# Performance work log

Hardware: AMD Instinct MI355X
Metric: run time of the kernel (lower is better)

## Reference

```python
import jax, jax.numpy as jnp
import numpy as np

B = 16384       # batch
H = 512         # hidden_size
OUT = 4         # output_size (== GRU input_size)
FF = 2048       # MLP hidden width
HORIZON = 5     # prediction_horizon


def setup_inputs() -> dict:
    key = jax.random.key(0)
    ks = jax.random.split(key, 12)
    s = 0.05
    f32 = jnp.float32
    return {
        "predicted_values": jax.random.normal(ks[0], (B, HORIZON, OUT), f32),
        "past_time_features": jax.random.normal(ks[1], (B, H), f32),
        # nn.GRU (single layer) params, PyTorch layout: (3H, in) / (3H, H), gate order r,z,n
        "w_ih": jax.random.normal(ks[2], (3 * H, OUT), f32) * s,
        "w_hh": jax.random.normal(ks[3], (3 * H, H), f32) * s,
        "b_ih": jax.random.normal(ks[4], (3 * H,), f32) * s,
        "b_hh": jax.random.normal(ks[5], (3 * H,), f32) * s,
        # hx_fc: Linear(2H -> H)
        "w_fc": jax.random.normal(ks[6], (H, 2 * H), f32) * s,
        "b_fc": jax.random.normal(ks[7], (H,), f32) * s,
        # mlp: Linear(H -> 2048), Linear(2048 -> OUT); Dropout is identity at eval
        "w1": jax.random.normal(ks[8], (FF, H), f32) * s,
        "b1": jax.random.normal(ks[9], (FF,), f32) * s,
        "w2": jax.random.normal(ks[10], (OUT, FF), f32) * s,
        "b2": jax.random.normal(ks[11], (OUT,), f32) * s,
    }


def _gru_cell(x, h, w_ih, w_hh, b_ih, b_hh):
    # PyTorch GRU cell: gates ordered (r, z, n)
    gi = x @ w_ih.T + b_ih          # [B, 3H]
    gh = h @ w_hh.T + b_hh          # [B, 3H]
    i_r, i_z, i_n = jnp.split(gi, 3, axis=-1)
    h_r, h_z, h_n = jnp.split(gh, 3, axis=-1)
    r = jax.nn.sigmoid(i_r + h_r)
    z = jax.nn.sigmoid(i_z + h_z)
    n = jnp.tanh(i_n + r * h_n)
    return (1.0 - z) * n + z * h


def reference(predicted_values, past_time_features, w_ih, w_hh, b_ih, b_hh,
              w_fc, b_fc, w1, b1, w2, b2):
    b = predicted_values.shape[0]
    xy = jnp.zeros((b, OUT), predicted_values.dtype)
    hx = past_time_features.reshape(b, H)
    outs = []
    for i in range(HORIZON):
        # length-2 sequence through the GRU: [xy, predicted_values[:, i]]
        h1 = _gru_cell(xy, hx, w_ih, w_hh, b_ih, b_hh)
        h2 = _gru_cell(predicted_values[:, i, :], h1, w_ih, w_hh, b_ih, b_hh)
        hcat = jnp.concatenate([h1, h2], axis=-1)        # [B, 2H]
        hx = hcat @ w_fc.T + b_fc                        # [B, H]
        # MLP: ReLU -> Linear -> (Dropout=identity) -> ReLU -> Linear
        d_xy = jax.nn.relu(jax.nn.relu(hx) @ w1.T + b1) @ w2.T + b2
        xy = xy + d_xy
        outs.append(xy)
    return jnp.stack(outs, axis=1)                       # [B, HORIZON, OUT]
```

## Files before the change

### kernel.cpp

```cpp
#include <hip/hip_runtime.h>
#include <hip/hip_bf16.h>
#include <cstdint>
#include <cstddef>

#define Bsz 16384
#define HORsz 5

using bf16_t = __hip_bfloat16;
typedef __bf16 bf16x8 __attribute__((ext_vector_type(8)));
typedef float f32x4 __attribute__((ext_vector_type(4)));

__device__ __forceinline__ void gld_lds16(const void* g, void* l) {
  __builtin_amdgcn_global_load_lds((__attribute__((address_space(1))) void*)g,
                                   (__attribute__((address_space(3))) void*)l,
                                   16, 0, 0);
}

__device__ __forceinline__ float sigm(float x) { return 1.f / (1.f + __expf(-x)); }
__device__ __forceinline__ float tanh_fast(float x) {
  x = fminf(fmaxf(x, -20.f), 20.f);
  float e = __expf(2.f * x);
  return (e - 1.f) / (e + 1.f);
}

template <int CTRL>
__device__ __forceinline__ float dpp_add(float v) {
  int x = __builtin_amdgcn_update_dpp(0, __float_as_int(v), CTRL, 0xF, 0xF, true);
  return v + __int_as_float(x);
}
__device__ __forceinline__ float red16(float v) {
  v = dpp_add<0xB1>(v);
  v = dpp_add<0x4E>(v);
  v = dpp_add<0x124>(v);
  v = dpp_add<0x128>(v);
  return v;
}

__device__ __forceinline__ void swz(int b, int nbn, int& n, int& m) {
  const int x = b & 7;
  const int k = b >> 3;
  n = k % nbn;
  m = x + 8 * (k / nbn);
}

__device__ __forceinline__ size_t fl_off(int row, int col, int ca, int cofs) {
  return (size_t)((row >> 4) * ca + cofs + (col >> 5)) * 1024
       + (size_t)((((col >> 3) & 3) * 16 + (row & 15)) * 16 + (col & 7) * 2);
}

__global__ void __launch_bounds__(256) pack_fl(const float* __restrict__ src,
                                               char* __restrict__ dst,
                                               int C, int cs, int npieces) {
  const int p = blockIdx.x * 256 + threadIdx.x;
  if (p >= npieces) return;
  const int chunk = p >> 6, wi = p & 63;
  const int colgrp = wi >> 4, r15 = wi & 15;
  const int rowgrp = chunk >> cs, kg = chunk & ((1 << cs) - 1);
  const int row = rowgrp * 16 + r15;
  const int col = kg * 32 + colgrp * 8;
  const float* s = src + (size_t)row * C + col;
  bf16x8 v;
  #pragma unroll
  for (int j = 0; j < 8; ++j) v[j] = (__bf16)s[j];
  *(bf16x8*)(dst + (size_t)p * 16) = v;
}

__global__ void __launch_bounds__(256) pack_x(const float* __restrict__ src, int ld,
                                              char* __restrict__ dst, int ntot) {
  const int p = blockIdx.x * 256 + threadIdx.x;
  if (p >= ntot) return;
  const int slice = p >> 14, row = p & 16383;
  const float* s = src + (size_t)row * ld + slice * 4;
  bf16x8 v;
  v[0] = (__bf16)s[0]; v[1] = (__bf16)s[1]; v[2] = (__bf16)s[2]; v[3] = (__bf16)s[3];
  v[4] = (__bf16)1.0f; v[5] = (__bf16)0.f; v[6] = (__bf16)0.f; v[7] = (__bf16)0.f;
  char* base = dst + (size_t)slice * 1048576 + (size_t)(row >> 4) * 1024 + (row & 15) * 16;
  const bf16x8 z = {};
  *(bf16x8*)(base) = v;
  *(bf16x8*)(base + 256) = z;
  *(bf16x8*)(base + 512) = z;
  *(bf16x8*)(base + 768) = z;
}

__global__ void __launch_bounds__(256) pack_wih(const float* __restrict__ w_ih,
                                                const float* __restrict__ b_ih,
                                                const float* __restrict__ b_hh,
                                                char* __restrict__ dst) {
  const int row = blockIdx.x * 256 + threadIdx.x;
  if (row >= 1536) return;
  const float* s = w_ih + (size_t)row * 4;
  const float c4 = b_ih[row] + (row < 1024 ? b_hh[row] : 0.f);
  bf16x8 v;
  v[0] = (__bf16)s[0]; v[1] = (__bf16)s[1]; v[2] = (__bf16)s[2]; v[3] = (__bf16)s[3];
  v[4] = (__bf16)c4;   v[5] = (__bf16)0.f; v[6] = (__bf16)0.f; v[7] = (__bf16)0.f;
  char* base = dst + (size_t)(row >> 4) * 1024 + (row & 15) * 16;
  const bf16x8 z = {};
  *(bf16x8*)(base) = v;
  *(bf16x8*)(base + 256) = z;
  *(bf16x8*)(base + 512) = z;
  *(bf16x8*)(base + 768) = z;
}

__global__ void __launch_bounds__(256, 3) gru_fused5(
    const char* __restrict__ Afl, int ca,
    const char* __restrict__ Wfl,
    const char* __restrict__ xF,
    const char* __restrict__ wihF,
    const float* __restrict__ b_hh,
    char* __restrict__ Ofl, int co, int kofs)
{
  __shared__ char smem[32768];
  const int t = threadIdx.x, w = t >> 6, lane = t & 63;
  int bn, bm;
  swz(blockIdx.x, 8, bn, bm);
  const int m0 = bm * 64;
  const int n0 = bn * 64;

  const char* gsrc[4];
  const char* gsrc16[4];
  int loff[4];
  #pragma unroll
  for (int s = 0; s < 4; ++s) {
    const int idx = w * 4 + s;
    if (idx < 4) {
      gsrc[s]   = Afl + (size_t)((m0 >> 4) + idx) * ca * 1024 + lane * 16;
      gsrc16[s] = xF  + (size_t)((m0 >> 4) + idx) * 1024 + lane * 16;
    } else {
      const int c = idx - 4, g = c >> 2, cr = c & 3;
      gsrc[s]   = Wfl  + (size_t)(g * 32 + (n0 >> 4) + cr) * 16 * 1024 + lane * 16;
      gsrc16[s] = wihF + (size_t)(g * 32 + (n0 >> 4) + cr) * 1024 + lane * 16;
    }
    loff[s] = idx * 1024;
  }

  f32x4 acc[3][4], acc_ni[4];
  const f32x4 zero = {0.f, 0.f, 0.f, 0.f};
  #pragma unroll
  for (int g = 0; g < 3; ++g)
    #pragma unroll
    for (int i = 0; i < 4; ++i) acc[g][i] = zero;
  #pragma unroll
  for (int i = 0; i < 4; ++i) acc_ni[i] = zero;

  #pragma unroll
  for (int s = 0; s < 4; ++s)
    gld_lds16(gsrc[s], smem + loff[s]);

  #pragma unroll
  for (int kg = 0; kg < 16; ++kg) {
    __syncthreads();
    const char* cur = smem + (kg & 1) * 16384;
    char* nxt = smem + ((kg + 1) & 1) * 16384;
    if (kg + 1 < 16) {
      #pragma unroll
      for (int s = 0; s < 4; ++s)
        gld_lds16(gsrc[s] + (size_t)(kg + 1) * 1024, nxt + loff[s]);
    } else {
      #pragma unroll
      for (int s = 0; s < 4; ++s)
        gld_lds16(gsrc16[s], nxt + loff[s]);
    }
    bf16x8 af[4];
    #pragma unroll
    for (int i = 0; i < 4; ++i)
      af[i] = *(const bf16x8*)(cur + i * 1024 + lane * 16);
    #pragma unroll
    for (int g = 0; g < 3; ++g) {
      const bf16x8 bv = *(const bf16x8*)(cur + (4 + g * 4 + w) * 1024 + lane * 16);
      #pragma unroll
      for (int i = 0; i < 4; ++i)
        acc[g][i] = __builtin_amdgcn_mfma_f32_16x16x32_bf16(af[i], bv, acc[g][i], 0, 0, 0);
    }
  }

  __syncthreads();
  {
    const char* cur = smem;
    bf16x8 af[4];
    #pragma unroll
    for (int i = 0; i < 4; ++i)
      af[i] = *(const bf16x8*)(cur + i * 1024 + lane * 16);
    #pragma unroll
    for (int g = 0; g < 2; ++g) {
      const bf16x8 bv = *(const bf16x8*)(cur + (4 + g * 4 + w) * 1024 + lane * 16);
      #pragma unroll
      for (int i = 0; i < 4; ++i)
        acc[g][i] = __builtin_amdgcn_mfma_f32_16x16x32_bf16(af[i], bv, acc[g][i], 0, 0, 0);
    }
    const bf16x8 bv2 = *(const bf16x8*)(cur + (4 + 8 + w) * 1024 + lane * 16);
    #pragma unroll
    for (int i = 0; i < 4; ++i)
      acc_ni[i] = __builtin_amdgcn_mfma_f32_16x16x32_bf16(af[i], bv2, acc_ni[i], 0, 0, 0);
  }
  __syncthreads();

  const int lr = lane & 15, q4 = (lane >> 4) * 4;
  char* rep = smem + w * 2048;
  const int c = n0 + w * 16 + lr;
  const float bhn = b_hh[c + 1024];
  const int wbase = ((lr >> 3) * 16 + q4) * 16 + (lr & 7) * 2;
  #pragma unroll
  for (int i = 0; i < 4; ++i) {
    #pragma unroll
    for (int r4 = 0; r4 < 4; ++r4) {
      const int row = m0 + i * 16 + q4 + r4;
      const float rr = sigm(acc[0][i][r4]);
      const float zz = sigm(acc[1][i][r4]);
      const float nn = tanh_fast(acc_ni[i][r4] + rr * (acc[2][i][r4] + bhn));
      const float hp = (float)*(const __bf16*)(Afl + fl_off(row, c, ca, 0));
      *(__bf16*)(rep + i * 512 + wbase + r4 * 16) = (__bf16)((1.f - zz) * nn + zz * hp);
    }
  }
  const int rg0 = m0 >> 4;
  const int cg = kofs + (n0 >> 5) + (w >> 1);
  const int half = (w & 1) * 512;
  #pragma unroll
  for (int i = 0; i < 4; ++i) {
    const uint2 v = *(const uint2*)(rep + i * 512 + lane * 8);
    *(uint2*)(Ofl + ((size_t)(rg0 + i) * co + cg) * 1024 + half + lane * 8) = v;
  }
}

template <int NKG, int NJ, int MODE>
__global__ void __launch_bounds__(256, 4) gemm_fl5(
    const char* __restrict__ Afl,
    const char* __restrict__ Bfl, int nbn,
    const float* __restrict__ bias,
    char* __restrict__ O1, char* __restrict__ O2, int co,
    const float* __restrict__ w2, float* __restrict__ dxy)
{
  constexpr int NCH = 8 + 2 * NJ;
  constexpr int NS = NCH / 4;
  constexpr int BUFB = NCH * 1024;
  __shared__ char smem[2 * BUFB];
  const int t = threadIdx.x, w = t >> 6, lane = t & 63;
  int bn, bm;
  swz(blockIdx.x, nbn, bn, bm);
  const int m0 = bm * 128, n0 = bn * (NJ * 32);
  const int wm = (w >> 1) * 64, wn = (w & 1) * (NJ * 16);

  const char* gsrc[NS];
  int loff[NS];
  #pragma unroll
  for (int s = 0; s < NS; ++s) {
    const int idx = w * NS + s;
    if (idx < 8) gsrc[s] = Afl + (size_t)((m0 >> 4) + idx) * NKG * 1024 + lane * 16;
    else         gsrc[s] = Bfl + (size_t)((n0 >> 4) + idx - 8) * NKG * 1024 + lane * 16;
    loff[s] = idx * 1024;
  }

  f32x4 acc[4][NJ];
  const f32x4 zero = {0.f, 0.f, 0.f, 0.f};
  #pragma unroll
  for (int i = 0; i < 4; ++i)
    #pragma unroll
    for (int j = 0; j < NJ; ++j) acc[i][j] = zero;

  #pragma unroll
  for (int s = 0; s < NS; ++s)
    gld_lds16(gsrc[s], smem + loff[s]);

  #pragma unroll
  for (int kg = 0; kg < NKG; ++kg) {
    __syncthreads();
    const char* cur = smem + (kg & 1) * BUFB;
    if (kg + 1 < NKG) {
      char* nxt = smem + ((kg + 1) & 1) * BUFB;
      #pragma unroll
      for (int s = 0; s < NS; ++s)
        gld_lds16(gsrc[s] + (size_t)(kg + 1) * 1024, nxt + loff[s]);
    }
    bf16x8 af[4], bv[NJ];
    #pragma unroll
    for (int i = 0; i < 4; ++i)
      af[i] = *(const bf16x8*)(cur + ((wm >> 4) + i) * 1024 + lane * 16);
    #pragma unroll
    for (int j = 0; j < NJ; ++j)
      bv[j] = *(const bf16x8*)(cur + (8 + (wn >> 4) + j) * 1024 + lane * 16);
    #pragma unroll
    for (int i = 0; i < 4; ++i)
      #pragma unroll
      for (int j = 0; j < NJ; ++j)
        acc[i][j] = __builtin_amdgcn_mfma_f32_16x16x32_bf16(af[i], bv[j], acc[i][j], 0, 0, 0);
  }

  const int lr = lane & 15, q4 = (lane >> 4) * 4;
  if (MODE == 2) {
    char* rep = smem + w * (NJ / 2) * 1024;
    const int rgb = (m0 >> 4) + (wm >> 4);
    const int cgb = (n0 >> 5) + (wn >> 5);
    for (int i = 0; i < 4; ++i) {
      #pragma unroll
      for (int j = 0; j < NJ; ++j) {
        const int col = n0 + wn + j * 16 + lr;
        const float bvv = bias[col];
        const int wbase = (((j & 1) * 2 + (lr >> 3)) * 16 + q4) * 16 + (lr & 7) * 2;
        #pragma unroll
        for (int r = 0; r < 4; ++r) {
          const float v = acc[i][j][r] + bvv;
          *(__bf16*)(rep + (j >> 1) * 1024 + wbase + r * 16) = (__bf16)v;
        }
      }
      #pragma unroll
      for (int jc = 0; jc < NJ / 2; ++jc) {
        const bf16x8 v = *(const bf16x8*)(rep + jc * 1024 + lane * 16);
        const size_t cb = ((size_t)(rgb + i) * co + cgb + jc) * 1024 + lane * 16;
        *(bf16x8*)(O1 + cb) = v;
        bf16x8 vr;
        #pragma unroll
        for (int e = 0; e < 8; ++e) vr[e] = (__bf16)fmaxf((float)v[e], 0.f);
        *(bf16x8*)(O2 + cb) = vr;
      }
    }
  }
}

__global__ void __launch_bounds__(512, 2) mlp2b(
    const char* __restrict__ Afl,
    const char* __restrict__ Bfl,
    const float* __restrict__ bias,
    const float* __restrict__ w2,
    float* __restrict__ dxy)
{
  __shared__ char smem[2 * 32768];
  const int t = threadIdx.x, w = t >> 6, lane = t & 63;
  const int wr = w >> 2, wc = w & 3;
  int bn, bm;
  swz(blockIdx.x, 8, bn, bm);
  const int m0 = bm * 256, n0 = bn * 256;

  const char* gsrc[4];
  int loff[4];
  #pragma unroll
  for (int s = 0; s < 4; ++s) {
    const int idx = w * 4 + s;
    if (idx < 16) {
      gsrc[s] = Afl + (size_t)((m0 >> 4) + idx) * 16 * 1024 + lane * 16;
      loff[s] = idx * 1024;
    } else {
      gsrc[s] = Bfl + (size_t)((n0 >> 4) + idx - 16) * 16 * 1024 + lane * 16;
      loff[s] = 16384 + (idx - 16) * 1024;
    }
  }

  f32x4 acc[8][4];
  const f32x4 zero = {0.f, 0.f, 0.f, 0.f};
  #pragma unroll
  for (int i = 0; i < 8; ++i)
    #pragma unroll
    for (int j = 0; j < 4; ++j) acc[i][j] = zero;

  #pragma unroll
  for (int s = 0; s < 4; ++s)
    gld_lds16(gsrc[s], smem + loff[s]);

  #pragma unroll
  for (int kg = 0; kg < 16; ++kg) {
    __syncthreads();
    const char* cur = smem + (kg & 1) * 32768;
    if (kg + 1 < 16) {
      char* nxt = smem + ((kg + 1) & 1) * 32768;
      #pragma unroll
      for (int s = 0; s < 4; ++s)
        gld_lds16(gsrc[s] + (size_t)(kg + 1) * 1024, nxt + loff[s]);
    }
    bf16x8 af[8], bv[4];
    #pragma unroll
    for (int j = 0; j < 4; ++j)
      bv[j] = *(const bf16x8*)(cur + 16384 + (wc * 4 + j) * 1024 + lane * 16);
    #pragma unroll
    for (int i = 0; i < 8; ++i)
      af[i] = *(const bf16x8*)(cur + (wr * 8 + i) * 1024 + lane * 16);
    __builtin_amdgcn_s_setprio(1);
    #pragma unroll
    for (int i = 0; i < 8; ++i)
      #pragma unroll
      for (int j = 0; j < 4; ++j)
        acc[i][j] = __builtin_amdgcn_mfma_f32_16x16x32_bf16(af[i], bv[j], acc[i][j], 0, 0, 0);
    __builtin_amdgcn_s_setprio(0);
  }

  const int lr = lane & 15, q4 = (lane >> 4) * 4;
  const int slice = bn * 4 + wc;
  float bvv[4], w2c[4][4];
  #pragma unroll
  for (int j = 0; j < 4; ++j) {
    const int col = n0 + wc * 64 + j * 16 + lr;
    bvv[j] = bias[col];
    w2c[j][0] = w2[col];        w2c[j][1] = w2[2048 + col];
    w2c[j][2] = w2[4096 + col]; w2c[j][3] = w2[6144 + col];
  }
  #pragma unroll
  for (int i = 0; i < 8; ++i) {
    float v[4][4];
    #pragma unroll
    for (int r = 0; r < 4; ++r)
      #pragma unroll
      for (int o = 0; o < 4; ++o) v[r][o] = 0.f;
    #pragma unroll
    for (int j = 0; j < 4; ++j) {
      #pragma unroll
      for (int r = 0; r < 4; ++r) {
        const float pv = fmaxf(acc[i][j][r] + bvv[j], 0.f);
        v[r][0] += pv * w2c[j][0]; v[r][1] += pv * w2c[j][1];
        v[r][2] += pv * w2c[j][2]; v[r][3] += pv * w2c[j][3];
      }
    }
    #pragma unroll
    for (int r = 0; r < 4; ++r)
      #pragma unroll
      for (int o = 0; o < 4; ++o) v[r][o] = red16(v[r][o]);
    if (lr == 0) {
      #pragma unroll
      for (int r = 0; r < 4; ++r) {
        const int row = m0 + wr * 128 + i * 16 + q4 + r;
        float4 vv = make_float4(v[r][0], v[r][1], v[r][2], v[r][3]);
        *(float4*)(dxy + ((size_t)slice * Bsz + row) * 4) = vv;
      }
    }
  }
}

__global__ void __launch_bounds__(256) finalize(
    const float* __restrict__ dxy, const float* __restrict__ b2,
    float* __restrict__ xy, float* __restrict__ out, int istep,
    char* __restrict__ xyF)
{
  const int b = blockIdx.x * 256 + threadIdx.x;
  float4 s = *(const float4*)b2;
  #pragma unroll 8
  for (int sl = 0; sl < 32; ++sl) {
    const float4 d = *(const float4*)(dxy + ((size_t)sl * Bsz + b) * 4);
    s.x += d.x; s.y += d.y; s.z += d.z; s.w += d.w;
  }
  float4 xv = *(const float4*)(xy + (size_t)b * 4);
  xv.x += s.x; xv.y += s.y; xv.z += s.z; xv.w += s.w;
  *(float4*)(xy + (size_t)b * 4) = xv;
  *(float4*)(out + (size_t)b * 20 + istep * 4) = xv;
  bf16x8 v;
  v[0] = (__bf16)xv.x; v[1] = (__bf16)xv.y; v[2] = (__bf16)xv.z; v[3] = (__bf16)xv.w;
  v[4] = (__bf16)1.0f; v[5] = (__bf16)0.f; v[6] = (__bf16)0.f; v[7] = (__bf16)0.f;
  *(bf16x8*)(xyF + (size_t)(b >> 4) * 1024 + (b & 15) * 16) = v;
}

extern "C" void kernel_launch(void* const* d_in, const int* in_sizes, int n_in,
                              void* d_out, int out_size, void* d_ws, size_t ws_size,
                              hipStream_t stream)
{
  const float* pv   = (const float*)d_in[0];
  const float* ptf  = (const float*)d_in[1];
  const float* w_ih = (const float*)d_in[2];
  const float* w_hh = (const float*)d_in[3];
  const float* b_ih = (const float*)d_in[4];
  const float* b_hh = (const float*)d_in[5];
  const float* w_fc = (const float*)d_in[6];
  const float* b_fc = (const float*)d_in[7];
  const float* w1   = (const float*)d_in[8];
  const float* b1   = (const float*)d_in[9];
  const float* w2   = (const float*)d_in[10];
  const float* b2   = (const float*)d_in[11];
  float* out = (float*)d_out;

  char* p = (char*)d_ws;
  auto carve = [&](size_t bytes) {
    char* r = p;
    p += (bytes + 255) & ~(size_t)255;
    return r;
  };
  char*  hxF   = carve((size_t)Bsz * 512 * 2);
  char*  hxrF  = carve((size_t)Bsz * 512 * 2);
  char*  hcatF = carve((size_t)Bsz * 1024 * 2);
  float* dxy   = (float*)carve((size_t)32 * Bsz * 4 * 4);
  float* xy    = (float*)carve((size_t)Bsz * 4 * 4);
  char*  whhF  = carve((size_t)1536 * 512 * 2);
  char*  wfcF  = carve((size_t)512 * 1024 * 2);
  char*  w1F   = carve((size_t)2048 * 512 * 2);
  char*  xyF   = carve((size_t)1024 * 1024);
  char*  pvF   = carve((size_t)5 * 1024 * 1024);
  char*  wihF  = carve((size_t)96 * 1024);

  pack_fl<<<(1536 * 512 / 8 + 255) / 256, 256, 0, stream>>>(w_hh, whhF, 512, 4, 1536 * 512 / 8);
  pack_fl<<<(512 * 1024 / 8 + 255) / 256, 256, 0, stream>>>(w_fc, wfcF, 1024, 5, 512 * 1024 / 8);
  pack_fl<<<(2048 * 512 / 8 + 255) / 256, 256, 0, stream>>>(w1, w1F, 512, 4, 2048 * 512 / 8);
  pack_fl<<<(Bsz * 512 / 8 + 255) / 256, 256, 0, stream>>>(ptf, hxF, 512, 4, Bsz * 512 / 8);
  pack_wih<<<6, 256, 0, stream>>>(w_ih, b_ih, b_hh, wihF);
  pack_x<<<(Bsz * HORsz + 255) / 256, 256, 0, stream>>>(pv, HORsz * 4, pvF, Bsz * HORsz);
  hipMemsetAsync(xy, 0, (size_t)Bsz * 4 * 4, stream);
  pack_x<<<Bsz / 256, 256, 0, stream>>>(xy, 4, xyF, Bsz);

  for (int i = 0; i < HORsz; ++i) {
    gru_fused5<<<2048, 256, 0, stream>>>(
        hxF, 16, whhF, xyF, wihF, b_hh, hcatF, 32, 0);
    gru_fused5<<<2048, 256, 0, stream>>>(
        hcatF, 32, whhF, pvF + (size_t)i * 1048576, wihF, b_hh, hcatF, 32, 16);
    gemm_fl5<32, 2, 2><<<1024, 256, 0, stream>>>(
        hcatF, wfcF, 8, b_fc, hxF, hxrF, 16, nullptr, nullptr);
    mlp2b<<<512, 512, 0, stream>>>(hxrF, w1F, b1, w2, dxy);
    finalize<<<Bsz / 256, 256, 0, stream>>>(dxy, b2, xy, out, i, xyF);
  }
}
```

Measured before the change: 863.8 us.

## Triple-buffer GRU GEMM LDS pipeline with vmcnt-based waits

Shared memory in the fused GRU kernel grows from two to three 16KB stages, and global-to-LDS loads are now issued two k-steps ahead. The full __syncthreads is replaced by `s_waitcnt vmcnt(4)` plus a raw barrier, so the load for the next stage can stay in flight while the current stage is consumed. The trailing barrier before the epilogue is dropped. The goal is to hide global load latency behind MFMA work. The cost is higher LDS use per block, which could limit occupancy, and the manual waitcnt logic is fragile.

```diff
diff --git a/kernel.cpp b/kernel.cpp
--- a/kernel.cpp
+++ b/kernel.cpp
@@ -14,6 +14,13 @@
   __builtin_amdgcn_global_load_lds((__attribute__((address_space(1))) void*)g,
                                    (__attribute__((address_space(3))) void*)l,
                                    16, 0, 0);
+}
+
+template <int N>
+__device__ __forceinline__ void wait_vmcnt() {
+  if constexpr (N == 0)      asm volatile("s_waitcnt vmcnt(0)" ::: "memory");
+  else if constexpr (N == 4) asm volatile("s_waitcnt vmcnt(4)" ::: "memory");
+  else static_assert(N == 0 || N == 4, "unsupported vmcnt");
 }
 
 __device__ __forceinline__ float sigm(float x) { return 1.f / (1.f + __expf(-x)); }
@@ -101,7 +108,7 @@
   *(bf16x8*)(base + 768) = z;
 }
 
-__global__ void __launch_bounds__(256, 3) gru_fused5(
+__global__ void __launch_bounds__(256, 3) gru_fused6(
     const char* __restrict__ Afl, int ca,
     const char* __restrict__ Wfl,
     const char* __restrict__ xF,
@@ -109,7 +116,7 @@
     const float* __restrict__ b_hh,
     char* __restrict__ Ofl, int co, int kofs)
 {
-  __shared__ char smem[32768];
+  __shared__ char smem[49152];
   const int t = threadIdx.x, w = t >> 6, lane = t & 63;
   int bn, bm;
   swz(blockIdx.x, 8, bn, bm);
@@ -145,20 +152,24 @@
   #pragma unroll
   for (int s = 0; s < 4; ++s)
     gld_lds16(gsrc[s], smem + loff[s]);
+  #pragma unroll
+  for (int s = 0; s < 4; ++s)
+    gld_lds16(gsrc[s] + 1024, smem + 16384 + loff[s]);
 
   #pragma unroll
   for (int kg = 0; kg < 16; ++kg) {
-    __syncthreads();
-    const char* cur = smem + (kg & 1) * 16384;
-    char* nxt = smem + ((kg + 1) & 1) * 16384;
-    if (kg + 1 < 16) {
-      #pragma unroll
-      for (int s = 0; s < 4; ++s)
-        gld_lds16(gsrc[s] + (size_t)(kg + 1) * 1024, nxt + loff[s]);
-    } else {
-      #pragma unroll
-      for (int s = 0; s < 4; ++s)
-        gld_lds16(gsrc16[s], nxt + loff[s]);
+    wait_vmcnt<4>();
+    __builtin_amdgcn_s_barrier();
+    __builtin_amdgcn_sched_barrier(0);
+    const char* cur = smem + (kg % 3) * 16384;
+    if (kg + 2 <= 16) {
+      char* nxt = smem + ((kg + 2) % 3) * 16384;
+      #pragma unroll
+      for (int s = 0; s < 4; ++s) {
+        const char* src = (kg + 2 < 16) ? gsrc[s] + (size_t)(kg + 2) * 1024
+                                        : gsrc16[s];
+        gld_lds16(src, nxt + loff[s]);
+      }
     }
     bf16x8 af[4];
     #pragma unroll
@@ -173,9 +184,11 @@
     }
   }
 
-  __syncthreads();
+  wait_vmcnt<0>();
+  __builtin_amdgcn_s_barrier();
+  __builtin_amdgcn_sched_barrier(0);
   {
-    const char* cur = smem;
+    const char* cur = smem + 16384;
     bf16x8 af[4];
     #pragma unroll
     for (int i = 0; i < 4; ++i)
@@ -192,7 +205,6 @@
     for (int i = 0; i < 4; ++i)
       acc_ni[i] = __builtin_amdgcn_mfma_f32_16x16x32_bf16(af[i], bv2, acc_ni[i], 0, 0, 0);
   }
-  __syncthreads();
 
   const int lr = lane & 15, q4 = (lane >> 4) * 4;
   char* rep = smem + w * 2048;
@@ -489,9 +501,9 @@
   pack_x<<<Bsz / 256, 256, 0, stream>>>(xy, 4, xyF, Bsz);
 
   for (int i = 0; i < HORsz; ++i) {
-    gru_fused5<<<2048, 256, 0, stream>>>(
+    gru_fused6<<<2048, 256, 0, stream>>>(
         hxF, 16, whhF, xyF, wihF, b_hh, hcatF, 32, 0);
-    gru_fused5<<<2048, 256, 0, stream>>>(
+    gru_fused6<<<2048, 256, 0, stream>>>(
         hcatF, 32, whhF, pvF + (size_t)i * 1048576, wihF, b_hh, hcatF, 32, 16);
     gemm_fl5<32, 2, 2><<<1024, 256, 0, stream>>>(
         hcatF, wfcF, 8, b_fc, hxF, hxrF, 16, nullptr, nullptr);
```

New measurement: 766.8 us. 11.2% less time.
